# Kernel tuning notes

Hardware: AMD Instinct MI355X
Metric: run time of the kernel (lower is better)

Reference implementation:

```python
import jax, jax.numpy as jnp
import numpy as np

N, D = 1024, 128
NEG_INF = -1e30


def setup_inputs() -> dict:
    key = jax.random.key(0)
    ks = jax.random.split(key, 8)
    s = 0.05
    return {
        "X": jax.random.normal(ks[0], (N, D), dtype=jnp.float32),
        "Wq": jax.random.normal(ks[1], (D, D), dtype=jnp.float32) * s,
        "Wk": jax.random.normal(ks[2], (D, D), dtype=jnp.float32) * s,
        "v": jax.random.normal(ks[3], (D,), dtype=jnp.float32) * s,
        "w_ih": jax.random.normal(ks[4], (3 * D, 2 * D), dtype=jnp.float32) * s,
        "w_hh": jax.random.normal(ks[5], (3 * D, D), dtype=jnp.float32) * s,
        "b_ih": jax.random.normal(ks[6], (3 * D,), dtype=jnp.float32) * s,
        "b_hh": jax.random.normal(ks[7], (3 * D,), dtype=jnp.float32) * s,
    }


def reference(X, Wq, Wk, v, w_ih, w_hh, b_ih, b_hh):
    n, d = X.shape
    # --- anti-causal additive attention (query i attends keys j >= i) ---
    q = X @ Wq.T                                   # (N, d)
    k = X @ Wk.T                                   # (N, d)
    # scores[i, j] = v . tanh(q_i + k_j)
    scores = jnp.einsum("ijd,d->ij", jnp.tanh(q[:, None, :] + k[None, :, :]), v)
    mask = jnp.arange(n)[None, :] >= jnp.arange(n)[:, None]   # suffix j >= i
    scores = jnp.where(mask, scores, NEG_INF)
    w = jax.nn.softmax(scores, axis=1)             # (N, N)
    att = w @ X                                    # (N, d) context over keys

    # --- single-layer GRU over the N "time" steps, batch 1 ---
    gru_in = jnp.concatenate((X, att), axis=1)     # (N, 2d)
    gi = gru_in @ w_ih.T + b_ih                    # (N, 3d) input gates, precomputed

    def step(h, gi_t):
        gh = h @ w_hh.T + b_hh                     # (3d,)
        i_r, i_z, i_n = jnp.split(gi_t, 3)
        h_r, h_z, h_n = jnp.split(gh, 3)
        r = jax.nn.sigmoid(i_r + h_r)
        z = jax.nn.sigmoid(i_z + h_z)
        nst = jnp.tanh(i_n + r * h_n)
        h_new = (1.0 - z) * nst + z * h
        return h_new, h_new

    h0 = jnp.zeros((d,), dtype=X.dtype)
    _, out = jax.lax.scan(step, h0, gi)            # (N, d)
    return out
```

## Files before the change

kernel.cpp:

```cpp
#include <hip/hip_runtime.h>
#include <hip/hip_bf16.h>

#define N 1024
#define D 128
#define SB 8
#define NSB (N / SB)

typedef __hip_bfloat16 bf16;
typedef __attribute__((ext_vector_type(8))) short bfx8;
typedef __attribute__((ext_vector_type(4))) float fx4;
typedef __attribute__((ext_vector_type(4))) unsigned short u16x4;

__device__ __forceinline__ float b2f(bf16 x) { return __bfloat162float(x); }
__device__ __forceinline__ short f2bf_bits(float x) {
    bf16 b = __float2bfloat16(x);
    return *reinterpret_cast<short*>(&b);
}
__device__ __forceinline__ float bfbits2f(unsigned short u) {
    return __uint_as_float(((unsigned int)u) << 16);
}
__device__ __forceinline__ float fastrcp(float x) { return __builtin_amdgcn_rcpf(x); }

__device__ __forceinline__ float fast_tanh(float x) {
    float e = __expf(2.f * x);
    return 1.f - 2.f * fastrcp(e + 1.f);
}
__device__ __forceinline__ float fast_sigmoid(float x) {
    return fastrcp(1.f + __expf(-x));
}

__device__ __forceinline__ float sel4(fx4 v, int r) {
    float x = (r & 1) ? v[1] : v[0];
    float y = (r & 1) ? v[3] : v[2];
    return (r & 2) ? y : x;
}

__device__ __forceinline__ void async_copy16(const float* g, void* l) {
    __builtin_amdgcn_global_load_lds((const __attribute__((address_space(1))) void*)g,
                                     (__attribute__((address_space(3))) void*)l, 16, 0, 0);
}

__device__ __forceinline__ void wait_rows(int* cnt, int grp) {
    while (__hip_atomic_load(&cnt[grp], __ATOMIC_ACQUIRE, __HIP_MEMORY_SCOPE_AGENT) < 8)
        __builtin_amdgcn_s_sleep(2);
}

__device__ __forceinline__ float cvt(const void* p, int idx, int isbf) {
    return isbf ? b2f(((const bf16*)p)[idx]) : ((const float*)p)[idx];
}

#define MFMA(A, B, C) __builtin_amdgcn_mfma_f32_16x16x32_bf16((A), (B), (C), 0, 0, 0)

__global__ void __launch_bounds__(256) prep_kernel(
        const void* inX, const void* inWq, const void* inWk, const void* inV,
        const void* inWih, const void* inWhh, const void* inBih, const void* inBhh,
        float* __restrict__ Xf, float* __restrict__ WqT, float* __restrict__ WkT,
        float* __restrict__ vf, float* __restrict__ wihT, float* __restrict__ whhf,
        float* __restrict__ bihf, float* __restrict__ bhhf,
        int* __restrict__ flag, int* __restrict__ cnt, int* __restrict__ rcnt) {
    __shared__ int red[256];
    int t = threadIdx.x;
    const unsigned short* xu = (const unsigned short*)inX;
    int c = 0;
#pragma unroll
    for (int k = 0; k < 4; ++k) {
        unsigned short u = xu[2 * (4 * t + k)];
        int e = (u >> 7) & 0xFF;
        c += (e >= 96 && e <= 144) ? 1 : 0;
    }
    red[t] = c;
    __syncthreads();
    for (int st = 128; st > 0; st >>= 1) {
        if (t < st) red[t] += red[t + st];
        __syncthreads();
    }
    int isbf = red[0] > 800;

    if (blockIdx.x == 0) {
        if (t == 0) *flag = isbf;
        if (t < 128) { cnt[t] = 0; rcnt[t] = 0; }
    }

    int id = blockIdx.x * 256 + t;
    if (id < 131072) {
        Xf[id] = cvt(inX, id, isbf);
    } else if (id < 147456) {
        int k = id - 131072; int cc = k >> 7, d = k & 127;
        WqT[k] = cvt(inWq, d * 128 + cc, isbf);
    } else if (id < 163840) {
        int k = id - 147456; int cc = k >> 7, d = k & 127;
        WkT[k] = cvt(inWk, d * 128 + cc, isbf);
    } else if (id < 163968) {
        vf[id - 163840] = cvt(inV, id - 163840, isbf);
    } else if (id < 262272) {
        int k = id - 163968; int cc = k / 384, o = k - cc * 384;
        wihT[k] = cvt(inWih, o * 256 + cc, isbf);
    } else if (id < 311424) {
        whhf[id - 262272] = cvt(inWhh, id - 262272, isbf);
    } else if (id < 311808) {
        bihf[id - 311424] = cvt(inBih, id - 311424, isbf);
    } else if (id < 312192) {
        bhhf[id - 311808] = cvt(inBhh, id - 311808, isbf);
    }
}

__global__ void __launch_bounds__(256) qk_gix_kernel(
        const float* __restrict__ X, const float* __restrict__ WqT,
        const float* __restrict__ WkT, const float* __restrict__ wihT,
        float* __restrict__ q, float* __restrict__ kT, float* __restrict__ gix) {
    int i = blockIdx.x, t = threadIdx.x;
    __shared__ float xs[D];
    if (t < D) xs[t] = X[i * D + t];
    __syncthreads();
    int d = t & 127;
    const float* WT = (t < 128) ? WqT : WkT;
    float acc = 0.f;
#pragma unroll 8
    for (int cc = 0; cc < D; ++cc) acc += xs[cc] * WT[cc * D + d];
    if (t < 128) q[i * D + d] = acc;
    else         kT[d * N + i] = acc;

    for (int o = t; o < 3 * D; o += 256) {
        float a2 = 0.f;
#pragma unroll 8
        for (int cc = 0; cc < D; ++cc) a2 += xs[cc] * wihT[cc * 384 + o];
        gix[i * 384 + o] = a2;
    }
}

__global__ void __launch_bounds__(256, 1) fused_kernel(
        const float* __restrict__ q, const float* __restrict__ kT,
        const float* __restrict__ v, const float* __restrict__ X,
        const float* __restrict__ wihTa, const float* __restrict__ b_ih,
        const float* __restrict__ b_hh, const float* __restrict__ gix,
        float* __restrict__ gi, const float* __restrict__ w_hh,
        void* __restrict__ out, const int* __restrict__ flag,
        int* __restrict__ cnt, int* __restrict__ rcnt,
        float* __restrict__ attMS, float* __restrict__ attA) {
    __shared__ __align__(16) char smem[2 * SB * 3 * D * 4 + (SB + 1) * D * 2];
    int t = threadIdx.x;

    if (blockIdx.x != 0) {
        int b = blockIdx.x - 1;
        int i, P, p;
        if (b < 256)      { i = b >> 3;            P = 8; p = b & 7; }
        else if (b < 448) { int e = b - 256; i = 32 + (e >> 1); P = 2; p = e & 1; }
        else              { i = 128 + (b - 448);   P = 1; p = 0; }

        float* qs   = (float*)smem;
        float* vs   = qs + D;
        float* al   = vs + D;
        float* wrow = al + D;
        float* red  = wrow + N;

        int len = (N - i + P - 1) / P;
        int j0 = i + p * len;
        int j1 = min(j0 + len, N);

        if (t < D) { qs[t] = q[i * D + t]; vs[t] = v[t]; }
        __syncthreads();

        float sj[4];
        float m = -1e30f;
#pragma unroll
        for (int it = 0; it < 4; ++it) {
            int j = j0 + t + it * 256;
            float s = -1e30f;
            if (j < j1) {
                s = 0.f;
#pragma unroll 8
                for (int dd = 0; dd < D; ++dd)
                    s += vs[dd] * fast_tanh(qs[dd] + kT[dd * N + j]);
            }
            sj[it] = s;
            m = fmaxf(m, s);
        }
        red[t] = m;
        __syncthreads();
        for (int st = 128; st > 0; st >>= 1) {
            if (t < st) red[t] = fmaxf(red[t], red[t + st]);
            __syncthreads();
        }
        m = red[0];
        __syncthreads();
        float lsum = 0.f;
#pragma unroll
        for (int it = 0; it < 4; ++it) {
            int j = j0 + t + it * 256;
            if (j < j1) {
                float pe = __expf(sj[it] - m);
                wrow[j - j0] = pe;
                lsum += pe;
            }
        }
        red[t] = lsum;
        __syncthreads();
        for (int st = 128; st > 0; st >>= 1) {
            if (t < st) red[t] += red[t + st];
            __syncthreads();
        }
        float S = red[0];
        __syncthreads();
        int d = t & 127, half = t >> 7;
        float acc = 0.f;
        int cl = j1 - j0;
#pragma unroll 4
        for (int jj = half; jj < cl; jj += 2) acc += wrow[jj] * X[(j0 + jj) * D + d];
        if (half) red[d] = acc;
        __syncthreads();
        if (!half) al[d] = acc + red[d];
        __syncthreads();

        if (P > 1) {
            if (t < D) attA[(i * 8 + p) * D + t] = al[t];
            if (t == 0) { attMS[(i * 8 + p) * 2] = m; attMS[(i * 8 + p) * 2 + 1] = S; }
            __syncthreads();
            if (t == 0) {
                __threadfence();
                int arr = __hip_atomic_fetch_add(&rcnt[i], 1, __ATOMIC_ACQ_REL,
                                                 __HIP_MEMORY_SCOPE_AGENT);
                ((int*)red)[0] = arr;
            }
            __syncthreads();
            int arr = ((int*)red)[0];
            if (arr != P - 1) return;
            if (t < D) {
                float M = -1e30f;
                for (int pp = 0; pp < P; ++pp) M = fmaxf(M, attMS[(i * 8 + pp) * 2]);
                float Ssum = 0.f, av = 0.f;
                for (int pp = 0; pp < P; ++pp) {
                    float wp = __expf(attMS[(i * 8 + pp) * 2] - M);
                    Ssum += attMS[(i * 8 + pp) * 2 + 1] * wp;
                    av += attA[(i * 8 + pp) * D + t] * wp;
                }
                al[t] = av * fastrcp(Ssum);
            }
            __syncthreads();
        } else {
            float inv = fastrcp(S);
            if (t < D) al[t] *= inv;
            __syncthreads();
        }

        for (int o = t; o < 3 * D; o += 256) {
            float a2 = b_ih[o] + ((o < 2 * D) ? b_hh[o] : 0.f) + gix[i * 384 + o];
            const float* wt = wihTa + o;
#pragma unroll 8
            for (int cc = 0; cc < D; ++cc) a2 += al[cc] * wt[cc * 384];
            gi[i * 3 * D + o] = a2;
        }
        __syncthreads();
        if (t == 0) {
            __threadfence();
            __hip_atomic_fetch_add(&cnt[i >> 3], 1, __ATOMIC_RELEASE, __HIP_MEMORY_SCOPE_AGENT);
        }
        return;
    }

    __builtin_amdgcn_s_setprio(2);
    float* gi_lds = (float*)smem;
    short* hist   = (short*)(smem + 2 * SB * 3 * D * 4);
    int w = t >> 6;
    int l = t & 63;
    int qq = l >> 4;
    int nn = l & 15;
    int isbf = *flag;

    bfx8 a[3][2][4];
#pragma unroll
    for (int tau = 0; tau < 3; ++tau)
#pragma unroll
        for (int mqi = 0; mqi < 2; ++mqi)
#pragma unroll
            for (int kc = 0; kc < 4; ++kc) {
                int row = 128 * tau + 16 * (2 * w + mqi) + nn;
                int k0 = 32 * kc + 8 * qq;
#pragma unroll
                for (int j = 0; j < 8; ++j)
                    a[tau][mqi][kc][j] = f2bf_bits(w_hh[row * D + k0 + j]);
            }
    fx4 bias2[2];
#pragma unroll
    for (int mqi = 0; mqi < 2; ++mqi)
#pragma unroll
        for (int r = 0; r < 4; ++r)
            bias2[mqi][r] = b_hh[2 * D + 16 * (2 * w + mqi) + 4 * qq + r];
    const fx4 zed = {0.f, 0.f, 0.f, 0.f};

    int rsel = l & 3;
    int mqsel = (l >> 3) & 1;
    int drow = 32 * w + 16 * mqsel + 4 * qq + rsel;
    float h = 0.f;

    int fr = 1 + (t >> 5);
    int fc = (t & 31) * 4;

    wait_rows(cnt, 0);
    {
        const float* src = gi;
        for (int mm = 0; mm < 3; ++mm) {
            int off = (w * 3 + mm) * 256;
            async_copy16(src + off + (l << 2), smem + off * 4);
        }
    }

    for (int sb = 0; sb < NSB; ++sb) {
        int cb = sb & 1;
        u16x4 hv = {0, 0, 0, 0};
        int hcopy = 0;
        if (sb > 0) {
            hv = *(const u16x4*)(hist + fr * D + fc);
            if (t < 64) hcopy = ((const int*)(hist + SB * D))[t];
        }
        if (sb + 1 < NSB) {
            wait_rows(cnt, sb + 1);
            const float* src = gi + (size_t)(sb + 1) * SB * 3 * D;
            char* dst = smem + (cb ^ 1) * SB * 3 * D * 4;
            for (int mm = 0; mm < 3; ++mm) {
                int off = (w * 3 + mm) * 256;
                async_copy16(src + off + (l << 2), dst + off * 4);
            }
        }
        if (sb > 0) {
            int orow = (sb - 1) * SB + fr - 1;
            if (isbf) {
                *(u16x4*)((unsigned short*)out + orow * D + fc) = hv;
            } else {
                float* op = (float*)out + orow * D + fc;
                fx4 f0;
#pragma unroll
                for (int j = 0; j < 4; ++j) f0[j] = bfbits2f(hv[j]);
                *(fx4*)op = f0;
            }
        }
        if (t < 64) ((int*)hist)[t] = (sb == 0) ? 0 : hcopy;

        if (sb == 0)
            asm volatile("s_waitcnt vmcnt(3) lgkmcnt(0)\ns_barrier" ::: "memory");
        else if (sb == 1)
            asm volatile("s_waitcnt vmcnt(4) lgkmcnt(0)\ns_barrier" ::: "memory");
        else if (sb + 1 < NSB)
            asm volatile("s_waitcnt vmcnt(5) lgkmcnt(0)\ns_barrier" ::: "memory");
        else
            asm volatile("s_waitcnt vmcnt(2) lgkmcnt(0)\ns_barrier" ::: "memory");

        const char* hrd = (const char*)hist + 16 * qq;
        const float* gp = gi_lds + cb * SB * 3 * D + drow;
        short* hwr = hist + D + drow;

        float gr = gp[0], gz = gp[D], gn = gp[2 * D];

        for (int s = 0; s < SB; ++s) {
            bfx8 b0 = *(const bfx8*)(hrd);
            bfx8 b1 = *(const bfx8*)(hrd + 64);
            bfx8 b2 = *(const bfx8*)(hrd + 128);
            bfx8 b3 = *(const bfx8*)(hrd + 192);
            float grn = 0.f, gzn = 0.f, gnn = 0.f;
            if (s + 1 < SB) {
                grn = gp[3 * D];
                gzn = gp[4 * D];
                gnn = gp[5 * D];
            }

            fx4 acc[3][2];
#pragma unroll
            for (int tau = 0; tau < 3; ++tau)
#pragma unroll
                for (int mqi = 0; mqi < 2; ++mqi) {
                    fx4 c0 = (tau == 2) ? bias2[mqi] : zed;
                    c0 = MFMA(a[tau][mqi][0], b0, c0);
                    c0 = MFMA(a[tau][mqi][1], b1, c0);
                    c0 = MFMA(a[tau][mqi][2], b2, c0);
                    c0 = MFMA(a[tau][mqi][3], b3, c0);
                    acc[tau][mqi] = c0;
                }

            float ar = sel4(mqsel ? acc[0][1] : acc[0][0], rsel);
            float az = sel4(mqsel ? acc[1][1] : acc[1][0], rsel);
            float an = sel4(mqsel ? acc[2][1] : acc[2][0], rsel);
            float rr = fast_sigmoid(gr + ar);
            float zz = fast_sigmoid(gz + az);
            float nst = fast_tanh(gn + rr * an);
            h = nst + zz * (h - nst);
            *hwr = f2bf_bits(h);

            hrd += 256;
            gp += 3 * D;
            hwr += D;
            gr = grn; gz = gzn; gn = gnn;
            asm volatile("s_waitcnt lgkmcnt(0)\ns_barrier" ::: "memory");
        }
    }
    {
        u16x4 hv = *(const u16x4*)(hist + fr * D + fc);
        int orow = (NSB - 1) * SB + fr - 1;
        if (isbf) {
            *(u16x4*)((unsigned short*)out + orow * D + fc) = hv;
        } else {
            float* op = (float*)out + orow * D + fc;
            fx4 f0;
#pragma unroll
            for (int j = 0; j < 4; ++j) f0[j] = bfbits2f(hv[j]);
            *(fx4*)op = f0;
        }
    }
}

extern "C" void kernel_launch(void* const* d_in, const int* in_sizes, int n_in,
                              void* d_out, int out_size, void* d_ws, size_t ws_size,
                              hipStream_t stream) {
    (void)in_sizes; (void)n_in; (void)out_size; (void)ws_size;

    float* w0 = (float*)d_ws;
    int*   flag = (int*)w0;
    int*   cnt  = (int*)w0 + 16;
    int*   rcnt = (int*)w0 + 160;
    float* base = w0 + 320;
    float* Xf    = base;
    float* vf    = Xf + 131072;
    float* whhf  = vf + 128;
    float* bihf  = whhf + 49152;
    float* bhhf  = bihf + 384;
    float* WqT   = bhhf + 384;
    float* WkT   = WqT + 16384;
    float* wihT  = WkT + 16384;
    float* q     = wihT + 98304;
    float* kT    = q + 131072;
    float* gix   = kT + 131072;
    float* gi    = gix + 393216;
    float* attMS = gi + 393216;
    float* attA  = attMS + 2048;

    prep_kernel<<<1220, 256, 0, stream>>>(d_in[0], d_in[1], d_in[2], d_in[3],
                                          d_in[4], d_in[5], d_in[6], d_in[7],
                                          Xf, WqT, WkT, vf, wihT, whhf, bihf, bhhf,
                                          flag, cnt, rcnt);
    qk_gix_kernel<<<N, 256, 0, stream>>>(Xf, WqT, WkT, wihT, q, kT, gix);
    fused_kernel<<<1345, 256, 0, stream>>>(q, kT, vf, Xf, wihT + 128 * 384, bihf, bhhf,
                                           gix, gi, whhf, d_out, flag, cnt, rcnt,
                                           attMS, attA);
}
```

Measured before the change: 555.2 us.

## Fuse prep and QK projection kernels; compute X-part of GRU input gates in attention blocks

Merges the conversion/prep kernel and the q/k/gix projection kernel into one launch. Each row block now converts X on the fly and stages transposed Wq/Wk chunks in shared memory instead of reading pre-transposed global copies. The X·w_ih contribution to the GRU input gates moves into the attention blocks of the fused kernel, which removes the gix buffer and one kernel launch. In exchange, every row block re-reads and re-converts the full Wq/Wk from the raw inputs, and the attention blocks do twice the gate matvec work.

Result: slower. 617.5 us (+11.2%).

```diff
diff --git a/kernel.cpp b/kernel.cpp
--- a/kernel.cpp
+++ b/kernel.cpp
@@ -5,6 +5,7 @@
 #define D 128
 #define SB 8
 #define NSB (N / SB)
+#define QK_NC 32
 
 typedef __hip_bfloat16 bf16;
 typedef __attribute__((ext_vector_type(8))) short bfx8;
@@ -51,15 +52,18 @@
 
 #define MFMA(A, B, C) __builtin_amdgcn_mfma_f32_16x16x32_bf16((A), (B), (C), 0, 0, 0)
 
-__global__ void __launch_bounds__(256) prep_kernel(
+__global__ void __launch_bounds__(256) qkprep_kernel(
         const void* inX, const void* inWq, const void* inWk, const void* inV,
         const void* inWih, const void* inWhh, const void* inBih, const void* inBhh,
-        float* __restrict__ Xf, float* __restrict__ WqT, float* __restrict__ WkT,
+        float* __restrict__ Xf, float* __restrict__ q, float* __restrict__ kT,
         float* __restrict__ vf, float* __restrict__ wihT, float* __restrict__ whhf,
         float* __restrict__ bihf, float* __restrict__ bhhf,
         int* __restrict__ flag, int* __restrict__ cnt, int* __restrict__ rcnt) {
+    __shared__ float xs[D];
     __shared__ int red[256];
-    int t = threadIdx.x;
+    __shared__ float stg[2][QK_NC][129];
+    int bid = blockIdx.x, t = threadIdx.x;
+
     const unsigned short* xu = (const unsigned short*)inX;
     int c = 0;
 #pragma unroll
@@ -76,63 +80,59 @@
     }
     int isbf = red[0] > 800;
 
-    if (blockIdx.x == 0) {
+    if (bid == 0) {
         if (t == 0) *flag = isbf;
         if (t < 128) { cnt[t] = 0; rcnt[t] = 0; }
     }
 
-    int id = blockIdx.x * 256 + t;
-    if (id < 131072) {
-        Xf[id] = cvt(inX, id, isbf);
-    } else if (id < 147456) {
-        int k = id - 131072; int cc = k >> 7, d = k & 127;
-        WqT[k] = cvt(inWq, d * 128 + cc, isbf);
-    } else if (id < 163840) {
-        int k = id - 147456; int cc = k >> 7, d = k & 127;
-        WkT[k] = cvt(inWk, d * 128 + cc, isbf);
-    } else if (id < 163968) {
-        vf[id - 163840] = cvt(inV, id - 163840, isbf);
-    } else if (id < 262272) {
-        int k = id - 163968; int cc = k / 384, o = k - cc * 384;
-        wihT[k] = cvt(inWih, o * 256 + cc, isbf);
-    } else if (id < 311424) {
-        whhf[id - 262272] = cvt(inWhh, id - 262272, isbf);
-    } else if (id < 311808) {
-        bihf[id - 311424] = cvt(inBih, id - 311424, isbf);
-    } else if (id < 312192) {
-        bhhf[id - 311808] = cvt(inBhh, id - 311808, isbf);
-    }
-}
-
-__global__ void __launch_bounds__(256) qk_gix_kernel(
-        const float* __restrict__ X, const float* __restrict__ WqT,
-        const float* __restrict__ WkT, const float* __restrict__ wihT,
-        float* __restrict__ q, float* __restrict__ kT, float* __restrict__ gix) {
-    int i = blockIdx.x, t = threadIdx.x;
-    __shared__ float xs[D];
-    if (t < D) xs[t] = X[i * D + t];
-    __syncthreads();
-    int d = t & 127;
-    const float* WT = (t < 128) ? WqT : WkT;
-    float acc = 0.f;
-#pragma unroll 8
-    for (int cc = 0; cc < D; ++cc) acc += xs[cc] * WT[cc * D + d];
-    if (t < 128) q[i * D + d] = acc;
-    else         kT[d * N + i] = acc;
-
-    for (int o = t; o < 3 * D; o += 256) {
-        float a2 = 0.f;
-#pragma unroll 8
-        for (int cc = 0; cc < D; ++cc) a2 += xs[cc] * wihT[cc * 384 + o];
-        gix[i * 384 + o] = a2;
+    if (bid < 1024) {
+        int i = bid;
+        if (t < D) {
+            float xv = cvt(inX, i * D + t, isbf);
+            xs[t] = xv;
+            Xf[i * D + t] = xv;
+        }
+        __syncthreads();
+        int d = t & 127;
+        float acc = 0.f;
+        for (int c0 = 0; c0 < D; c0 += QK_NC) {
+            for (int e = t; e < 2 * 128 * QK_NC; e += 256) {
+                int w = e >> 12;
+                int r = e & 4095;
+                int dd = r >> 5;
+                int cc = r & 31;
+                stg[w][cc][dd] = cvt(w ? inWk : inWq, dd * D + c0 + cc, isbf);
+            }
+            __syncthreads();
+            const float (*S)[129] = (t < 128) ? stg[0] : stg[1];
+#pragma unroll
+            for (int cc = 0; cc < QK_NC; ++cc) acc += xs[c0 + cc] * S[cc][d];
+            __syncthreads();
+        }
+        if (t < 128) q[i * D + d] = acc;
+        else         kT[d * N + i] = acc;
+    } else {
+        int id = (bid - 1024) * 256 + t;
+        if (id < 128) {
+            vf[id] = cvt(inV, id, isbf);
+        } else if (id < 98432) {
+            int k = id - 128; int cc = k / 384, o = k - cc * 384;
+            wihT[k] = cvt(inWih, o * 256 + cc, isbf);
+        } else if (id < 147584) {
+            whhf[id - 98432] = cvt(inWhh, id - 98432, isbf);
+        } else if (id < 147968) {
+            bihf[id - 147584] = cvt(inBih, id - 147584, isbf);
+        } else if (id < 148352) {
+            bhhf[id - 147968] = cvt(inBhh, id - 147968, isbf);
+        }
     }
 }
 
 __global__ void __launch_bounds__(256, 1) fused_kernel(
         const float* __restrict__ q, const float* __restrict__ kT,
         const float* __restrict__ v, const float* __restrict__ X,
-        const float* __restrict__ wihTa, const float* __restrict__ b_ih,
-        const float* __restrict__ b_hh, const float* __restrict__ gix,
+        const float* __restrict__ wihT, const float* __restrict__ b_ih,
+        const float* __restrict__ b_hh,
         float* __restrict__ gi, const float* __restrict__ w_hh,
         void* __restrict__ out, const int* __restrict__ flag,
         int* __restrict__ cnt, int* __restrict__ rcnt,
@@ -149,7 +149,8 @@
 
         float* qs   = (float*)smem;
         float* vs   = qs + D;
-        float* al   = vs + D;
+        float* xr   = vs + D;
+        float* al   = xr + D;
         float* wrow = al + D;
         float* red  = wrow + N;
 
@@ -157,7 +158,7 @@
         int j0 = i + p * len;
         int j1 = min(j0 + len, N);
 
-        if (t < D) { qs[t] = q[i * D + t]; vs[t] = v[t]; }
+        if (t < D) { qs[t] = q[i * D + t]; vs[t] = v[t]; xr[t] = X[i * D + t]; }
         __syncthreads();
 
         float sj[4];
@@ -243,10 +244,13 @@
         }
 
         for (int o = t; o < 3 * D; o += 256) {
-            float a2 = b_ih[o] + ((o < 2 * D) ? b_hh[o] : 0.f) + gix[i * 384 + o];
-            const float* wt = wihTa + o;
+            float a2 = b_ih[o] + ((o < 2 * D) ? b_hh[o] : 0.f);
+            const float* wtx = wihT + o;
+            const float* wta = wihT + 128 * 384 + o;
 #pragma unroll 8
-            for (int cc = 0; cc < D; ++cc) a2 += al[cc] * wt[cc * 384];
+            for (int cc = 0; cc < D; ++cc) a2 += xr[cc] * wtx[cc * 384];
+#pragma unroll 8
+            for (int cc = 0; cc < D; ++cc) a2 += al[cc] * wta[cc * 384];
             gi[i * 3 * D + o] = a2;
         }
         __syncthreads();
@@ -421,22 +425,18 @@
     float* whhf  = vf + 128;
     float* bihf  = whhf + 49152;
     float* bhhf  = bihf + 384;
-    float* WqT   = bhhf + 384;
-    float* WkT   = WqT + 16384;
-    float* wihT  = WkT + 16384;
+    float* wihT  = bhhf + 384;
     float* q     = wihT + 98304;
     float* kT    = q + 131072;
-    float* gix   = kT + 131072;
-    float* gi    = gix + 393216;
+    float* gi    = kT + 131072;
     float* attMS = gi + 393216;
     float* attA  = attMS + 2048;
 
-    prep_kernel<<<1220, 256, 0, stream>>>(d_in[0], d_in[1], d_in[2], d_in[3],
-                                          d_in[4], d_in[5], d_in[6], d_in[7],
-                                          Xf, WqT, WkT, vf, wihT, whhf, bihf, bhhf,
-                                          flag, cnt, rcnt);
-    qk_gix_kernel<<<N, 256, 0, stream>>>(Xf, WqT, WkT, wihT, q, kT, gix);
-    fused_kernel<<<1345, 256, 0, stream>>>(q, kT, vf, Xf, wihT + 128 * 384, bihf, bhhf,
-                                           gix, gi, whhf, d_out, flag, cnt, rcnt,
+    qkprep_kernel<<<1604, 256, 0, stream>>>(d_in[0], d_in[1], d_in[2], d_in[3],
+                                            d_in[4], d_in[5], d_in[6], d_in[7],
+                                            Xf, q, kT, vf, wihT, whhf, bihf, bhhf,
+                                            flag, cnt, rcnt);
+    fused_kernel<<<1345, 256, 0, stream>>>(q, kT, vf, Xf, wihT, bihf, bhhf,
+                                           gi, whhf, d_out, flag, cnt, rcnt,
                                            attMS, attA);
 }
```
